# Kernel tuning notes

Measured on AMD Instinct MI355X. Metric: run time of the kernel, lower is better.

The kernel has to match this reference:

```python
import jax, jax.numpy as jnp
import numpy as np

B, S, H = 2, 512, 768
NH, HD = 12, 64  # num heads, head size


def setup_inputs() -> dict:
    key = jax.random.key(0)
    ks = jax.random.split(key, 11)
    std = 0.02
    return {
        "from_path_hidden": jax.random.normal(ks[0], (B, S, H), jnp.float32),
        "to_path_hidden": jax.random.normal(ks[1], (B, S, H), jnp.float32),
        "attention_mask": jnp.zeros((B, 1, 1, S), jnp.float32),
        "Wq": jax.random.normal(ks[2], (H, H), jnp.float32) * std,
        "bq": jnp.zeros((H,), jnp.float32),
        "Wk": jax.random.normal(ks[3], (H, H), jnp.float32) * std,
        "bk": jnp.zeros((H,), jnp.float32),
        "Wvf": jax.random.normal(ks[4], (H, H), jnp.float32) * std,
        "bvf": jnp.zeros((H,), jnp.float32),
        "Wvt": jax.random.normal(ks[5], (H, H), jnp.float32) * std,
        "bvt": jnp.zeros((H,), jnp.float32),
    }


def _heads(x):
    # [B,S,H] -> [B,NH,S,HD]
    b, s, _ = x.shape
    return x.reshape(b, s, NH, HD).transpose(0, 2, 1, 3)


def reference(from_path_hidden, to_path_hidden, attention_mask,
              Wq, bq, Wk, bk, Wvf, bvf, Wvt, bvt):
    # torch Linear: y = x @ W^T + b
    q = _heads(from_path_hidden @ Wq.T + bq)   # [B,NH,S,HD]
    k = _heads(to_path_hidden @ Wk.T + bk)     # [B,NH,S,HD]
    vf = _heads(from_path_hidden @ Wvf.T + bvf)  # value_from, indexed by query pos
    vt = _heads(to_path_hidden @ Wvt.T + bvt)    # value_to, indexed by key pos

    scores = jnp.einsum("bhqd,bhkd->bhqk", q, k) / jnp.sqrt(jnp.asarray(HD, q.dtype))
    scores = scores + attention_mask  # additive mask, broadcasts [B,1,1,S]
    probs = jax.nn.softmax(scores, axis=-1)  # dropout is identity in eval mode

    # use_expanded_value=True: ctx[b,h,q,:] = sum_k probs[b,h,q,k] * (vf[b,h,q,:] + vt[b,h,k,:])
    # = probs @ vt + (sum_k probs) * vf  -- exact, avoids the [B,NH,S,S,HD] tensor
    ctx = jnp.einsum("bhqk,bhkd->bhqd", probs, vt) + probs.sum(-1, keepdims=True) * vf

    # [B,NH,S,HD] -> [B,S,H]
    ctx = ctx.transpose(0, 2, 1, 3).reshape(from_path_hidden.shape[0], -1, NH * HD)
    return ctx
```

## Files before the change

### kernel.cpp

```cpp
#include <hip/hip_runtime.h>
#include <hip/hip_bf16.h>
#include <math.h>

#define Bq  2
#define Sq  512
#define Hq  768
#define NHq 12
#define HDq 64
#define SHsz (Bq * Sq * Hq)
#define WSZ  (Hq * Hq)

typedef __bf16 bf16x8 __attribute__((ext_vector_type(8)));
typedef unsigned short u16x8 __attribute__((ext_vector_type(8)));
typedef float f32x4 __attribute__((ext_vector_type(4)));

static __device__ __forceinline__ unsigned short f2bf(float f) {
    unsigned int u = __float_as_uint(f);
    u += 0x7fffu + ((u >> 16) & 1u);
    return (unsigned short)(u >> 16);
}

static __device__ __forceinline__ f32x4 mfma_bf16(bf16x8 a, bf16x8 b, f32x4 c) {
    return __builtin_amdgcn_mfma_f32_16x16x32_bf16(a, b, c, 0, 0, 0);
}

static __device__ __forceinline__ void async16(const void* g, void* l) {
    __builtin_amdgcn_global_load_lds(
        (const __attribute__((address_space(1))) void*)(uintptr_t)g,
        (__attribute__((address_space(3))) void*)(unsigned int)(uintptr_t)l,
        16, 0, 0);
}

__global__ __launch_bounds__(256) void cvt_kernel(
    const float* __restrict__ from_h, const float* __restrict__ to_h,
    const float* __restrict__ Wq, const float* __restrict__ Wk,
    const float* __restrict__ Wvf, const float* __restrict__ Wvt,
    unsigned short* __restrict__ ws)
{
    const int z = blockIdx.y;
    const float* src; unsigned short* dst; int n;
    switch (z) {
        case 0:  src = from_h; dst = ws + 3 * SHsz;           n = SHsz; break;
        case 1:  src = to_h;   dst = ws + 4 * SHsz;           n = SHsz; break;
        case 2:  src = Wq;     dst = ws + 5 * SHsz;           n = WSZ;  break;
        case 3:  src = Wk;     dst = ws + 5 * SHsz + WSZ;     n = WSZ;  break;
        case 4:  src = Wvf;    dst = ws + 5 * SHsz + 2 * WSZ; n = WSZ;  break;
        default: src = Wvt;    dst = ws + 5 * SHsz + 3 * WSZ; n = WSZ;  break;
    }
    const int idx = (blockIdx.x * 256 + threadIdx.x) * 8;
    if (idx < n) {
        const float4 a = *(const float4*)(src + idx);
        const float4 b = *(const float4*)(src + idx + 4);
        u16x8 o = { f2bf(a.x), f2bf(a.y), f2bf(a.z), f2bf(a.w),
                    f2bf(b.x), f2bf(b.y), f2bf(b.z), f2bf(b.w) };
        *(u16x8*)(dst + idx) = o;
    }
}

__global__ __launch_bounds__(256) void proj_gemm(
    const unsigned short* __restrict__ fbf, const unsigned short* __restrict__ tbf,
    const unsigned short* __restrict__ wqb, const unsigned short* __restrict__ wkb,
    const unsigned short* __restrict__ wvfb, const unsigned short* __restrict__ wvtb,
    const float* __restrict__ bq, const float* __restrict__ bk,
    const float* __restrict__ bvf, const float* __restrict__ bvt,
    unsigned short* __restrict__ qbf, unsigned short* __restrict__ kbf,
    unsigned short* __restrict__ vtt, float* __restrict__ outp)
{
    __shared__ unsigned short lds[8192];
    unsigned short* Als = lds;
    unsigned short* Wls = lds + 4096;

    const int z = blockIdx.z;
    const unsigned short *A, *W;
    const float* bias;
    if (z == 0)      { A = fbf; W = wqb;  bias = bq;  }
    else if (z == 1) { A = tbf; W = wkb;  bias = bk;  }
    else if (z == 2) { A = tbf; W = wvtb; bias = bvt; }
    else             { A = fbf; W = wvfb; bias = bvf; }

    const int t    = threadIdx.x;
    const int wv   = t >> 6;
    const int lane = t & 63;
    const int l16  = lane & 15;
    const int quad = lane >> 4;
    const int bn = blockIdx.x;
    const int bm = blockIdx.y;

    const int srow = lane >> 3;
    const int sgrp = (lane & 7) ^ (srow & 7);

    f32x4 acc[4] = {};

    for (int kt = 0; kt < Hq / 64; ++kt) {
        __syncthreads();
        #pragma unroll
        for (int c = 0; c < 2; ++c) {
            const int r0 = wv * 16 + c * 8;
            const unsigned short* ga = A + (size_t)(bm * 64 + r0 + srow) * Hq + kt * 64 + sgrp * 8;
            async16(ga, &Als[r0 * 64]);
            const unsigned short* gw = W + (size_t)(bn * 64 + r0 + srow) * Hq + kt * 64 + sgrp * 8;
            async16(gw, &Wls[r0 * 64]);
        }
        __syncthreads();

        #pragma unroll
        for (int kk = 0; kk < 2; ++kk) {
            const int sg = ((kk * 4 + quad) ^ (l16 & 7)) * 8;
            const bf16x8 af = *(const bf16x8*)&Als[(wv * 16 + l16) * 64 + sg];
            #pragma unroll
            for (int j = 0; j < 4; ++j) {
                const bf16x8 bfr = *(const bf16x8*)&Wls[(j * 16 + l16) * 64 + sg];
                acc[j] = mfma_bf16(af, bfr, acc[j]);
            }
        }
    }

    __syncthreads();

    if (z == 3) {
        #pragma unroll
        for (int j = 0; j < 4; ++j) {
            const int ncol = bn * 64 + j * 16 + l16;
            const float bv = bias[ncol];
            #pragma unroll
            for (int r = 0; r < 4; ++r) {
                const int m = bm * 64 + wv * 16 + quad * 4 + r;
                outp[(size_t)m * Hq + ncol] = acc[j][r] + bv;
            }
        }
        return;
    }

    unsigned short* rep = lds;
    if (z == 2) {
        #pragma unroll
        for (int j = 0; j < 4; ++j) {
            const float bv = bias[bn * 64 + j * 16 + l16];
            #pragma unroll
            for (int r = 0; r < 4; ++r)
                rep[(j * 16 + l16) * 72 + wv * 16 + quad * 4 + r] = f2bf(acc[j][r] + bv);
        }
    } else {
        #pragma unroll
        for (int j = 0; j < 4; ++j) {
            const float bv = bias[bn * 64 + j * 16 + l16];
            #pragma unroll
            for (int r = 0; r < 4; ++r)
                rep[(wv * 16 + quad * 4 + r) * 72 + j * 16 + l16] = f2bf(acc[j][r] + bv);
        }
    }
    __syncthreads();

    const int row = t >> 2;
    #pragma unroll
    for (int p = 0; p < 2; ++p) {
        const int col0 = ((t & 3) + p * 4) * 8;
        const u16x8 v = *(const u16x8*)&rep[row * 72 + col0];
        if (z == 2) {
            const int bb = bm >> 3, m0 = (bm & 7) * 64;
            *(u16x8*)&vtt[((size_t)((bb * NHq + bn) * HDq + row)) * Sq + m0 + col0] = v;
        } else {
            unsigned short* dstp = (z == 0) ? qbf : kbf;
            *(u16x8*)&dstp[(size_t)(bm * 64 + row) * Hq + bn * 64 + col0] = v;
        }
    }
}

__global__ __launch_bounds__(64) void attn_kernel(
    const unsigned short* __restrict__ qbf,
    const unsigned short* __restrict__ kbf,
    const unsigned short* __restrict__ vtt,
    const float* __restrict__ amask,
    float* __restrict__ outp)
{
    __shared__ unsigned short Plds[16 * 40];

    const int t    = threadIdx.x;
    const int l16  = t & 15;
    const int quad = t >> 4;
    const int qt = blockIdx.x;
    const int h  = blockIdx.y;
    const int b  = blockIdx.z;
    const int q0 = qt * 16;

    const unsigned short* qrow = qbf + ((size_t)(b * Sq + q0 + l16)) * Hq + h * HDq + quad * 8;
    const bf16x8 aq0 = *(const bf16x8*)qrow;
    const bf16x8 aq1 = *(const bf16x8*)(qrow + 32);

    f32x4 O[4] = {};
    float ts[4] = {0.f, 0.f, 0.f, 0.f};
    const float scale = 0.125f;

    for (int kt = 0; kt < Sq / 32; ++kt) {
        const int k0 = kt * 32;
        const unsigned short* kr = kbf + ((size_t)(b * Sq + k0 + l16)) * Hq + h * HDq + quad * 8;
        const bf16x8 kb00 = *(const bf16x8*)kr;
        const bf16x8 kb01 = *(const bf16x8*)(kr + 32);
        const bf16x8 kb10 = *(const bf16x8*)(kr + 16 * Hq);
        const bf16x8 kb11 = *(const bf16x8*)(kr + 16 * Hq + 32);

        f32x4 s0 = {}, s1 = {};
        s0 = mfma_bf16(aq0, kb00, s0);
        s0 = mfma_bf16(aq1, kb01, s0);
        s1 = mfma_bf16(aq0, kb10, s1);
        s1 = mfma_bf16(aq1, kb11, s1);

        const float mk0 = amask[b * Sq + k0 + l16];
        const float mk1 = amask[b * Sq + k0 + 16 + l16];

        float p0[4], p1[4];
        #pragma unroll
        for (int r = 0; r < 4; ++r) {
            p0[r] = __expf(s0[r] * scale + mk0);
            p1[r] = __expf(s1[r] * scale + mk1);
            ts[r] += p0[r] + p1[r];
        }

        #pragma unroll
        for (int r = 0; r < 4; ++r) {
            Plds[(quad * 4 + r) * 40 + l16]      = f2bf(p0[r]);
            Plds[(quad * 4 + r) * 40 + 16 + l16] = f2bf(p1[r]);
        }
        const bf16x8 pa = *(const bf16x8*)&Plds[l16 * 40 + quad * 8];

        const unsigned short* vr = vtt + ((size_t)((b * NHq + h) * HDq + l16)) * Sq + k0 + quad * 8;
        #pragma unroll
        for (int j = 0; j < 4; ++j) {
            const bf16x8 vb = *(const bf16x8*)(vr + (size_t)j * 16 * Sq);
            O[j] = mfma_bf16(pa, vb, O[j]);
        }
    }

    #pragma unroll
    for (int off = 1; off < 16; off <<= 1) {
        #pragma unroll
        for (int r = 0; r < 4; ++r) ts[r] += __shfl_xor(ts[r], off);
    }

    #pragma unroll
    for (int r = 0; r < 4; ++r) {
        const float inv = 1.f / ts[r];
        const int row = q0 + quad * 4 + r;
        #pragma unroll
        for (int j = 0; j < 4; ++j) {
            const int col = h * HDq + j * 16 + l16;
            outp[((size_t)(b * Sq + row)) * Hq + col] += O[j][r] * inv;
        }
    }
}

extern "C" void kernel_launch(void* const* d_in, const int* in_sizes, int n_in,
                              void* d_out, int out_size, void* d_ws, size_t ws_size,
                              hipStream_t stream) {
    (void)in_sizes; (void)n_in; (void)out_size; (void)ws_size;
    const float* from_h = (const float*)d_in[0];
    const float* to_h   = (const float*)d_in[1];
    const float* amask  = (const float*)d_in[2];
    const float* Wq  = (const float*)d_in[3];
    const float* bqv = (const float*)d_in[4];
    const float* Wk  = (const float*)d_in[5];
    const float* bkv = (const float*)d_in[6];
    const float* Wvf = (const float*)d_in[7];
    const float* bvf = (const float*)d_in[8];
    const float* Wvt = (const float*)d_in[9];
    const float* bvt = (const float*)d_in[10];
    float* outp = (float*)d_out;

    unsigned short* ws = (unsigned short*)d_ws;
    unsigned short* qbf = ws;
    unsigned short* kbf = ws + SHsz;
    unsigned short* vtt = ws + 2 * SHsz;
    unsigned short* fbf = ws + 3 * SHsz;
    unsigned short* tbf = ws + 4 * SHsz;
    unsigned short* wqb  = ws + 5 * SHsz;
    unsigned short* wkb  = wqb + WSZ;
    unsigned short* wvfb = wqb + 2 * WSZ;
    unsigned short* wvtb = wqb + 3 * WSZ;

    cvt_kernel<<<dim3(384, 6), 256, 0, stream>>>(from_h, to_h, Wq, Wk, Wvf, Wvt, ws);

    dim3 gp(12, 16, 4);
    proj_gemm<<<gp, 256, 0, stream>>>(fbf, tbf, wqb, wkb, wvfb, wvtb,
                                      bqv, bkv, bvf, bvt, qbf, kbf, vtt, outp);

    dim3 ga(Sq / 16, NHq, Bq);
    attn_kernel<<<ga, 64, 0, stream>>>(qbf, kbf, vtt, amask, outp);
}
```

Baseline: 111.0 us.

## Enlarge projection GEMM M-tile and double-buffer K loads in attention

```diff
diff --git a/kernel.cpp b/kernel.cpp
--- a/kernel.cpp
+++ b/kernel.cpp
@@ -66,9 +66,9 @@
     unsigned short* __restrict__ qbf, unsigned short* __restrict__ kbf,
     unsigned short* __restrict__ vtt, float* __restrict__ outp)
 {
-    __shared__ unsigned short lds[8192];
+    __shared__ unsigned short lds[12288];
     unsigned short* Als = lds;
-    unsigned short* Wls = lds + 4096;
+    unsigned short* Wls = lds + 8192;
 
     const int z = blockIdx.z;
     const unsigned short *A, *W;
@@ -89,28 +89,35 @@
     const int srow = lane >> 3;
     const int sgrp = (lane & 7) ^ (srow & 7);
 
-    f32x4 acc[4] = {};
+    f32x4 acc[2][4] = {};
 
     for (int kt = 0; kt < Hq / 64; ++kt) {
         __syncthreads();
         #pragma unroll
+        for (int c = 0; c < 4; ++c) {
+            const int r0 = wv * 32 + c * 8;
+            async16(A + (size_t)(bm * 128 + r0 + srow) * Hq + kt * 64 + sgrp * 8, &Als[r0 * 64]);
+        }
+        #pragma unroll
         for (int c = 0; c < 2; ++c) {
             const int r0 = wv * 16 + c * 8;
-            const unsigned short* ga = A + (size_t)(bm * 64 + r0 + srow) * Hq + kt * 64 + sgrp * 8;
-            async16(ga, &Als[r0 * 64]);
-            const unsigned short* gw = W + (size_t)(bn * 64 + r0 + srow) * Hq + kt * 64 + sgrp * 8;
-            async16(gw, &Wls[r0 * 64]);
+            async16(W + (size_t)(bn * 64 + r0 + srow) * Hq + kt * 64 + sgrp * 8, &Wls[r0 * 64]);
         }
         __syncthreads();
 
         #pragma unroll
         for (int kk = 0; kk < 2; ++kk) {
             const int sg = ((kk * 4 + quad) ^ (l16 & 7)) * 8;
-            const bf16x8 af = *(const bf16x8*)&Als[(wv * 16 + l16) * 64 + sg];
+            bf16x8 af[2];
+            #pragma unroll
+            for (int i = 0; i < 2; ++i)
+                af[i] = *(const bf16x8*)&Als[(wv * 32 + i * 16 + l16) * 64 + sg];
             #pragma unroll
             for (int j = 0; j < 4; ++j) {
                 const bf16x8 bfr = *(const bf16x8*)&Wls[(j * 16 + l16) * 64 + sg];
-                acc[j] = mfma_bf16(af, bfr, acc[j]);
+                #pragma unroll
+                for (int i = 0; i < 2; ++i)
+                    acc[i][j] = mfma_bf16(af[i], bfr, acc[i][j]);
             }
         }
     }
@@ -123,10 +130,12 @@
             const int ncol = bn * 64 + j * 16 + l16;
             const float bv = bias[ncol];
             #pragma unroll
-            for (int r = 0; r < 4; ++r) {
-                const int m = bm * 64 + wv * 16 + quad * 4 + r;
-                outp[(size_t)m * Hq + ncol] = acc[j][r] + bv;
-            }
+            for (int i = 0; i < 2; ++i)
+                #pragma unroll
+                for (int r = 0; r < 4; ++r) {
+                    const int m = bm * 128 + wv * 32 + i * 16 + quad * 4 + r;
+                    outp[(size_t)m * Hq + ncol] = acc[i][j][r] + bv;
+                }
         }
         return;
     }
@@ -137,31 +146,38 @@
         for (int j = 0; j < 4; ++j) {
             const float bv = bias[bn * 64 + j * 16 + l16];
             #pragma unroll
-            for (int r = 0; r < 4; ++r)
-                rep[(j * 16 + l16) * 72 + wv * 16 + quad * 4 + r] = f2bf(acc[j][r] + bv);
+            for (int i = 0; i < 2; ++i)
+                #pragma unroll
+                for (int r = 0; r < 4; ++r)
+                    rep[(j * 16 + l16) * 136 + wv * 32 + i * 16 + quad * 4 + r] = f2bf(acc[i][j][r] + bv);
+        }
+        __syncthreads();
+        const int row = t >> 2;
+        const int bb = bm >> 2, m0 = (bm & 3) * 128;
+        #pragma unroll
+        for (int p = 0; p < 4; ++p) {
+            const int g = (t & 3) + p * 4;
+            const u16x8 v = *(const u16x8*)&rep[row * 136 + g * 8];
+            *(u16x8*)&vtt[((size_t)((bb * NHq + bn) * HDq + row)) * Sq + m0 + g * 8] = v;
         }
     } else {
         #pragma unroll
         for (int j = 0; j < 4; ++j) {
             const float bv = bias[bn * 64 + j * 16 + l16];
             #pragma unroll
-            for (int r = 0; r < 4; ++r)
-                rep[(wv * 16 + quad * 4 + r) * 72 + j * 16 + l16] = f2bf(acc[j][r] + bv);
-        }
-    }
-    __syncthreads();
-
-    const int row = t >> 2;
-    #pragma unroll
-    for (int p = 0; p < 2; ++p) {
-        const int col0 = ((t & 3) + p * 4) * 8;
-        const u16x8 v = *(const u16x8*)&rep[row * 72 + col0];
-        if (z == 2) {
-            const int bb = bm >> 3, m0 = (bm & 7) * 64;
-            *(u16x8*)&vtt[((size_t)((bb * NHq + bn) * HDq + row)) * Sq + m0 + col0] = v;
-        } else {
-            unsigned short* dstp = (z == 0) ? qbf : kbf;
-            *(u16x8*)&dstp[(size_t)(bm * 64 + row) * Hq + bn * 64 + col0] = v;
+            for (int i = 0; i < 2; ++i)
+                #pragma unroll
+                for (int r = 0; r < 4; ++r)
+                    rep[(wv * 32 + i * 16 + quad * 4 + r) * 72 + j * 16 + l16] = f2bf(acc[i][j][r] + bv);
+        }
+        __syncthreads();
+        unsigned short* dstp = (z == 0) ? qbf : kbf;
+        const int row = t >> 1;
+        #pragma unroll
+        for (int p = 0; p < 4; ++p) {
+            const int g = (t & 1) * 4 + p;
+            const u16x8 v = *(const u16x8*)&rep[row * 72 + g * 8];
+            *(u16x8*)&dstp[(size_t)(bm * 128 + row) * Hq + bn * 64 + g * 8] = v;
         }
     }
 }
@@ -173,69 +189,90 @@
     const float* __restrict__ amask,
     float* __restrict__ outp)
 {
-    __shared__ unsigned short Plds[16 * 40];
+    __shared__ unsigned short Plds[16 * 72];
 
     const int t    = threadIdx.x;
     const int l16  = t & 15;
     const int quad = t >> 4;
-    const int qt = blockIdx.x;
+    const int q0 = blockIdx.x * 16;
     const int h  = blockIdx.y;
     const int b  = blockIdx.z;
-    const int q0 = qt * 16;
 
     const unsigned short* qrow = qbf + ((size_t)(b * Sq + q0 + l16)) * Hq + h * HDq + quad * 8;
     const bf16x8 aq0 = *(const bf16x8*)qrow;
     const bf16x8 aq1 = *(const bf16x8*)(qrow + 32);
 
+    const unsigned short* kbase = kbf + ((size_t)(b * Sq + l16)) * Hq + h * HDq + quad * 8;
+    const unsigned short* vbase = vtt + ((size_t)((b * NHq + h) * HDq + l16)) * Sq + quad * 8;
+
     f32x4 O[4] = {};
     float ts[4] = {0.f, 0.f, 0.f, 0.f};
     const float scale = 0.125f;
 
-    for (int kt = 0; kt < Sq / 32; ++kt) {
-        const int k0 = kt * 32;
-        const unsigned short* kr = kbf + ((size_t)(b * Sq + k0 + l16)) * Hq + h * HDq + quad * 8;
-        const bf16x8 kb00 = *(const bf16x8*)kr;
-        const bf16x8 kb01 = *(const bf16x8*)(kr + 32);
-        const bf16x8 kb10 = *(const bf16x8*)(kr + 16 * Hq);
-        const bf16x8 kb11 = *(const bf16x8*)(kr + 16 * Hq + 32);
-
-        f32x4 s0 = {}, s1 = {};
-        s0 = mfma_bf16(aq0, kb00, s0);
-        s0 = mfma_bf16(aq1, kb01, s0);
-        s1 = mfma_bf16(aq0, kb10, s1);
-        s1 = mfma_bf16(aq1, kb11, s1);
-
-        const float mk0 = amask[b * Sq + k0 + l16];
-        const float mk1 = amask[b * Sq + k0 + 16 + l16];
-
-        float p0[4], p1[4];
-        #pragma unroll
-        for (int r = 0; r < 4; ++r) {
-            p0[r] = __expf(s0[r] * scale + mk0);
-            p1[r] = __expf(s1[r] * scale + mk1);
-            ts[r] += p0[r] + p1[r];
-        }
-
-        #pragma unroll
-        for (int r = 0; r < 4; ++r) {
-            Plds[(quad * 4 + r) * 40 + l16]      = f2bf(p0[r]);
-            Plds[(quad * 4 + r) * 40 + 16 + l16] = f2bf(p1[r]);
-        }
-        const bf16x8 pa = *(const bf16x8*)&Plds[l16 * 40 + quad * 8];
-
-        const unsigned short* vr = vtt + ((size_t)((b * NHq + h) * HDq + l16)) * Sq + k0 + quad * 8;
-        #pragma unroll
-        for (int j = 0; j < 4; ++j) {
-            const bf16x8 vb = *(const bf16x8*)(vr + (size_t)j * 16 * Sq);
-            O[j] = mfma_bf16(pa, vb, O[j]);
-        }
-    }
-
+    bf16x8 kb[2][4][2];
     #pragma unroll
-    for (int off = 1; off < 16; off <<= 1) {
+    for (int kg = 0; kg < 4; ++kg) {
+        kb[0][kg][0] = *(const bf16x8*)(kbase + (size_t)(kg * 16) * Hq);
+        kb[0][kg][1] = *(const bf16x8*)(kbase + (size_t)(kg * 16) * Hq + 32);
+    }
+
+    #pragma unroll
+    for (int kt = 0; kt < Sq / 64; ++kt) {
+        const int cur = kt & 1, nxt = cur ^ 1;
+        const int k0 = kt * 64;
+
+        f32x4 s[4] = {};
+        #pragma unroll
+        for (int kg = 0; kg < 4; ++kg) {
+            s[kg] = mfma_bf16(aq0, kb[cur][kg][0], s[kg]);
+            s[kg] = mfma_bf16(aq1, kb[cur][kg][1], s[kg]);
+        }
+
+        if (kt < Sq / 64 - 1) {
+            #pragma unroll
+            for (int kg = 0; kg < 4; ++kg) {
+                kb[nxt][kg][0] = *(const bf16x8*)(kbase + (size_t)(k0 + 64 + kg * 16) * Hq);
+                kb[nxt][kg][1] = *(const bf16x8*)(kbase + (size_t)(k0 + 64 + kg * 16) * Hq + 32);
+            }
+        }
+
+        bf16x8 vb[4][2];
+        #pragma unroll
+        for (int j = 0; j < 4; ++j) {
+            vb[j][0] = *(const bf16x8*)(vbase + (size_t)(j * 16) * Sq + k0);
+            vb[j][1] = *(const bf16x8*)(vbase + (size_t)(j * 16) * Sq + k0 + 32);
+        }
+
+        float p[4][4];
+        #pragma unroll
+        for (int kg = 0; kg < 4; ++kg) {
+            const float mk = amask[b * Sq + k0 + kg * 16 + l16];
+            #pragma unroll
+            for (int r = 0; r < 4; ++r) {
+                p[kg][r] = __expf(s[kg][r] * scale + mk);
+                ts[r] += p[kg][r];
+            }
+        }
+
+        #pragma unroll
+        for (int kg = 0; kg < 4; ++kg)
+            #pragma unroll
+            for (int r = 0; r < 4; ++r)
+                Plds[(quad * 4 + r) * 72 + kg * 16 + l16] = f2bf(p[kg][r]);
+        const bf16x8 pa0 = *(const bf16x8*)&Plds[l16 * 72 + quad * 8];
+        const bf16x8 pa1 = *(const bf16x8*)&Plds[l16 * 72 + 32 + quad * 8];
+
+        #pragma unroll
+        for (int j = 0; j < 4; ++j) {
+            O[j] = mfma_bf16(pa0, vb[j][0], O[j]);
+            O[j] = mfma_bf16(pa1, vb[j][1], O[j]);
+        }
+    }
+
+    #pragma unroll
+    for (int off = 1; off < 16; off <<= 1)
         #pragma unroll
         for (int r = 0; r < 4; ++r) ts[r] += __shfl_xor(ts[r], off);
-    }
 
     #pragma unroll
     for (int r = 0; r < 4; ++r) {
@@ -279,7 +316,7 @@
 
     cvt_kernel<<<dim3(384, 6), 256, 0, stream>>>(from_h, to_h, Wq, Wk, Wvf, Wvt, ws);
 
-    dim3 gp(12, 16, 4);
+    dim3 gp(12, 8, 4);
     proj_gemm<<<gp, 256, 0, stream>>>(fbf, tbf, wqb, wkb, wvfb, wvtb,
                                       bqv, bkv, bvf, bvt, qbf, kbf, vtt, outp);
 
```

New measurement: 115.5 us. +4.1%, slower.

## Split attention key range across two waves per block and merge partials via LDS

Applied to the files above, without the earlier changes.

```diff
diff --git a/kernel.cpp b/kernel.cpp
--- a/kernel.cpp
+++ b/kernel.cpp
@@ -96,10 +96,8 @@
         #pragma unroll
         for (int c = 0; c < 2; ++c) {
             const int r0 = wv * 16 + c * 8;
-            const unsigned short* ga = A + (size_t)(bm * 64 + r0 + srow) * Hq + kt * 64 + sgrp * 8;
-            async16(ga, &Als[r0 * 64]);
-            const unsigned short* gw = W + (size_t)(bn * 64 + r0 + srow) * Hq + kt * 64 + sgrp * 8;
-            async16(gw, &Wls[r0 * 64]);
+            async16(A + (size_t)(bm * 64 + r0 + srow) * Hq + kt * 64 + sgrp * 8, &Als[r0 * 64]);
+            async16(W + (size_t)(bn * 64 + r0 + srow) * Hq + kt * 64 + sgrp * 8, &Wls[r0 * 64]);
         }
         __syncthreads();
 
@@ -166,22 +164,25 @@
     }
 }
 
-__global__ __launch_bounds__(64) void attn_kernel(
+__global__ __launch_bounds__(128) void attn_kernel(
     const unsigned short* __restrict__ qbf,
     const unsigned short* __restrict__ kbf,
     const unsigned short* __restrict__ vtt,
     const float* __restrict__ amask,
     float* __restrict__ outp)
 {
-    __shared__ unsigned short Plds[16 * 40];
+    __shared__ unsigned short Plds[2 * 16 * 40];
+    __shared__ float Ols[16 * 68];
+    __shared__ float Tls[16];
 
     const int t    = threadIdx.x;
-    const int l16  = t & 15;
-    const int quad = t >> 4;
-    const int qt = blockIdx.x;
+    const int wv   = t >> 6;
+    const int lane = t & 63;
+    const int l16  = lane & 15;
+    const int quad = lane >> 4;
+    const int q0 = blockIdx.x * 16;
     const int h  = blockIdx.y;
     const int b  = blockIdx.z;
-    const int q0 = qt * 16;
 
     const unsigned short* qrow = qbf + ((size_t)(b * Sq + q0 + l16)) * Hq + h * HDq + quad * 8;
     const bf16x8 aq0 = *(const bf16x8*)qrow;
@@ -190,9 +191,10 @@
     f32x4 O[4] = {};
     float ts[4] = {0.f, 0.f, 0.f, 0.f};
     const float scale = 0.125f;
-
-    for (int kt = 0; kt < Sq / 32; ++kt) {
-        const int k0 = kt * 32;
+    unsigned short* myP = &Plds[wv * 16 * 40];
+
+    for (int kt = 0; kt < 8; ++kt) {
+        const int k0 = wv * 256 + kt * 32;
         const unsigned short* kr = kbf + ((size_t)(b * Sq + k0 + l16)) * Hq + h * HDq + quad * 8;
         const bf16x8 kb00 = *(const bf16x8*)kr;
         const bf16x8 kb01 = *(const bf16x8*)(kr + 32);
@@ -218,10 +220,10 @@
 
         #pragma unroll
         for (int r = 0; r < 4; ++r) {
-            Plds[(quad * 4 + r) * 40 + l16]      = f2bf(p0[r]);
-            Plds[(quad * 4 + r) * 40 + 16 + l16] = f2bf(p1[r]);
-        }
-        const bf16x8 pa = *(const bf16x8*)&Plds[l16 * 40 + quad * 8];
+            myP[(quad * 4 + r) * 40 + l16]      = f2bf(p0[r]);
+            myP[(quad * 4 + r) * 40 + 16 + l16] = f2bf(p1[r]);
+        }
+        const bf16x8 pa = *(const bf16x8*)&myP[l16 * 40 + quad * 8];
 
         const unsigned short* vr = vtt + ((size_t)((b * NHq + h) * HDq + l16)) * Sq + k0 + quad * 8;
         #pragma unroll
@@ -232,19 +234,33 @@
     }
 
     #pragma unroll
-    for (int off = 1; off < 16; off <<= 1) {
+    for (int off = 1; off < 16; off <<= 1)
         #pragma unroll
         for (int r = 0; r < 4; ++r) ts[r] += __shfl_xor(ts[r], off);
-    }
+
+    if (wv == 1) {
+        #pragma unroll
+        for (int j = 0; j < 4; ++j)
+            #pragma unroll
+            for (int r = 0; r < 4; ++r)
+                Ols[(quad * 4 + r) * 68 + j * 16 + l16] = O[j][r];
+        if (l16 == 0)
+            #pragma unroll
+            for (int r = 0; r < 4; ++r) Tls[quad * 4 + r] = ts[r];
+    }
+    __syncthreads();
+    if (wv == 1) return;
 
     #pragma unroll
     for (int r = 0; r < 4; ++r) {
-        const float inv = 1.f / ts[r];
+        const float l = ts[r] + Tls[quad * 4 + r];
+        const float inv = 1.f / l;
         const int row = q0 + quad * 4 + r;
         #pragma unroll
         for (int j = 0; j < 4; ++j) {
             const int col = h * HDq + j * 16 + l16;
-            outp[((size_t)(b * Sq + row)) * Hq + col] += O[j][r] * inv;
+            const float oj = O[j][r] + Ols[(quad * 4 + r) * 68 + j * 16 + l16];
+            outp[((size_t)(b * Sq + row)) * Hq + col] += oj * inv;
         }
     }
 }
@@ -284,5 +300,5 @@
                                       bqv, bkv, bvf, bvt, qbf, kbf, vtt, outp);
 
     dim3 ga(Sq / 16, NHq, Bq);
-    attn_kernel<<<ga, 64, 0, stream>>>(qbf, kbf, vtt, amask, outp);
-}
+    attn_kernel<<<ga, 128, 0, stream>>>(qbf, kbf, vtt, amask, outp);
+}
```

New measurement: 108.1 us. 2.6% less time.
